# Optimization experiments

Hardware: AMD Instinct MI355X
Metric: run time of the kernel (lower is better)

Reference implementation:

```python
import jax, jax.numpy as jnp
import numpy as np

NDIM = 3
N = 192
DX = 1.0 / N          # uniform unit box
T_REF = 300.0         # reference temperature [K]
MU_REF = 1.8e-5       # reference viscosity [Pa s]
PR = 0.72             # Prandtl number
CP = 1005.0           # specific heat [J/kg/K]


def _ddx(f, axis):
    # 2nd-order central difference, periodic BC
    return (jnp.roll(f, -1, axis) - jnp.roll(f, 1, axis)) / (2.0 * DX)


def _gradient(f):
    # scalar [N,N,N] -> [NDIM, N,N,N]
    return jnp.stack([_ddx(f, a) for a in range(NDIM)], axis=0)


def _divergence(v):
    # vector [NDIM, N,N,N] -> [N,N,N]
    out = _ddx(v[0], 0)
    for a in range(1, NDIM):
        out = out + _ddx(v[a], a)
    return out


def _viscosity(T_dim):
    return MU_REF * (T_dim / T_REF) ** 0.7


def _conductivity(T_dim):
    return _viscosity(T_dim) * CP / PR


def setup_inputs() -> dict:
    key = jax.random.key(0)
    k1, k2 = jax.random.split(key)
    u = jax.random.normal(k1, (NDIM, N, N, N), dtype=jnp.float32)
    # nondimensional temperature, kept positive for the power-law viscosity
    T = jax.random.uniform(k2, (N, N, N), dtype=jnp.float32, minval=0.5, maxval=1.5)
    return {"u": u, "T": T}


def reference(u, T):
    # --- stress tensor ---
    mu = _viscosity(T * T_REF)                                   # [N,N,N]
    # gradu[i, j] = d u_i / d x_j
    gradu = jnp.stack([_gradient(u[i]) for i in range(NDIM)], 0)  # [3,3,N,N,N]
    divu = jnp.einsum('ii...->...', gradu)                        # trace -> [N,N,N]
    S = 0.5 * (gradu + jnp.swapaxes(gradu, 0, 1))                 # symmetrized
    eye = jnp.eye(NDIM, dtype=u.dtype)[:, :, None, None, None]
    tau = 2.0 * mu * S - (2.0 / 3.0) * mu * divu * eye            # [3,3,N,N,N]

    # --- heat flux ---
    k = _conductivity(T * T_REF)
    heat_flux = -k * _gradient(T)                                 # [3,N,N,N]

    # --- assemble RHS: [mass(=0), momentum(3), energy] ---
    momentum = jnp.stack([_divergence(tau[i]) for i in range(NDIM)], 0)
    energy = -_divergence(heat_flux)
    for i in range(NDIM):
        energy = energy + _divergence(tau[i] * u[i])
    zero = jnp.zeros_like(T)
    return jnp.concatenate([zero[None], momentum, energy[None]], axis=0)
```

## Files before the change

### kernel.cpp

```cpp
#include <hip/hip_runtime.h>

#define N  192
#define N2 (N * N)
#define N3 (N * N * N)

#define TX 32
#define TY 8
#define NT 256
#define ZC 12
#define GX (N / TX)
#define GY (N / TY)
#define GZ (N / ZC)
#define NBLK (GX * GY * GZ)
#define UX (TX + 4)
#define UY (TY + 4)
#define UP (UX * UY)
#define FX (TX + 2)
#define FY (TY + 2)
#define FP (FX * FY)

static constexpr float INV2DX     = (float)N / 2.0f;
static constexpr float MU_REF_F   = 1.8e-5f;
static constexpr float CP_OVER_PR = 1005.0f / 0.72f;
static constexpr float TWO_THIRDS = 2.0f / 3.0f;

__device__ __forceinline__ int wrapN(int a) {
    if (a < 0)  a += N;
    if (a >= N) a -= N;
    return a;
}

struct Flux { float t00, t01, t02, t11, t12, t22, F0, F1, F2; };

__device__ __forceinline__ Flux flux_eval(const float4* __restrict__ uM,
                                          const float4* __restrict__ uC,
                                          const float4* __restrict__ uP,
                                          int c)
{
    const float4 cc = uC[c];
    const float4 xp = uC[c + 1],  xm = uC[c - 1];
    const float4 yp = uC[c + UX], ym = uC[c - UX];
    const float4 zp = uP[c],      zm = uM[c];

    const float d00 = (zp.x - zm.x) * INV2DX;
    const float d01 = (yp.x - ym.x) * INV2DX;
    const float d02 = (xp.x - xm.x) * INV2DX;
    const float d10 = (zp.y - zm.y) * INV2DX;
    const float d11 = (yp.y - ym.y) * INV2DX;
    const float d12 = (xp.y - xm.y) * INV2DX;
    const float d20 = (zp.z - zm.z) * INV2DX;
    const float d21 = (yp.z - ym.z) * INV2DX;
    const float d22 = (xp.z - xm.z) * INV2DX;
    const float dT0 = (zp.w - zm.w) * INV2DX;
    const float dT1 = (yp.w - ym.w) * INV2DX;
    const float dT2 = (xp.w - xm.w) * INV2DX;

    const float mu   = MU_REF_F * __powf(cc.w, 0.7f);
    const float divu = d00 + d11 + d22;
    const float lam  = -TWO_THIRDS * mu * divu;

    Flux f;
    f.t00 = 2.0f * mu * d00 + lam;
    f.t11 = 2.0f * mu * d11 + lam;
    f.t22 = 2.0f * mu * d22 + lam;
    f.t01 = mu * (d01 + d10);
    f.t02 = mu * (d02 + d20);
    f.t12 = mu * (d12 + d21);
    const float kc = mu * CP_OVER_PR;
    f.F0 = kc * dT0 + f.t00 * cc.x + f.t01 * cc.y + f.t02 * cc.z;
    f.F1 = kc * dT1 + f.t01 * cc.x + f.t11 * cc.y + f.t12 * cc.z;
    f.F2 = kc * dT2 + f.t02 * cc.x + f.t12 * cc.y + f.t22 * cc.z;
    return f;
}

__device__ __forceinline__ void sf_store(float4* __restrict__ sA, float4* __restrict__ sB,
                                         int fi, const Flux& f)
{
    sA[fi] = make_float4(f.t01, f.t02, f.t11, f.t12);
    sB[fi] = make_float4(f.t22, f.F1,  f.F2,  0.0f);
}

__global__ __launch_bounds__(NT)
void diffusion_zmarch_kernel(const float* __restrict__ u,
                             const float* __restrict__ Tp,
                             float* __restrict__ out)
{
    __shared__ float4 su4[4][UP];
    __shared__ float4 sfA[2][FP];
    __shared__ float4 sfB[2][FP];

    const int id  = (int)blockIdx.x;
    const int nid = (id & 7) * (NBLK / 8) + (id >> 3);
    const int bzB = nid / (GX * GY);
    const int rem = nid % (GX * GY);
    const int bx  = (rem % GX) * TX;
    const int by  = (rem / GX) * TY;
    const int z0  = bzB * ZC;

    const int tx  = threadIdx.x & (TX - 1);
    const int ty  = threadIdx.x >> 5;
    const int tid = (int)threadIdx.x;

    const float* __restrict__ u0 = u;
    const float* __restrict__ u1 = u + N3;
    const float* __restrict__ u2 = u + 2 * N3;

    const int cu = (ty + 2) * UX + (tx + 2);
    const int fi = (ty + 1) * FX + (tx + 1);

    int hfx = -1, hfy = -1;
    if (tid < TX)                 { hfy = 0;      hfx = 1 + tid; }
    else if (tid < 2 * TX)        { hfy = FY - 1; hfx = 1 + tid - TX; }
    else if (tid < 2 * TX + TY)   { hfx = 0;      hfy = 1 + tid - 2 * TX; }
    else if (tid < 2 * (TX + TY)) { hfx = FX - 1; hfy = 1 + tid - 2 * TX - TY; }
    const int hcu = (hfy + 1) * UX + (hfx + 1);
    const int hfi = hfy * FX + hfx;

    const int  q0   = tid;
    const int  q1   = tid + NT;
    const bool has2 = (q1 < UP);
    int ro0, ro1 = 0;
    {
        const int ux = q0 % UX, uy = q0 / UX;
        ro0 = wrapN(by + uy - 2) * N + wrapN(bx + ux - 2);
    }
    if (has2) {
        const int ux = q1 % UX, uy = q1 / UX;
        ro1 = wrapN(by + uy - 2) * N + wrapN(bx + ux - 2);
    }

#define STAGE_DIRECT(slot, zw)                                              \
    do {                                                                    \
        const int base_ = (zw) * N2;                                        \
        {  const int g_ = base_ + ro0;                                      \
           su4[slot][q0] = make_float4(u0[g_], u1[g_], u2[g_], Tp[g_]); }   \
        if (has2) {                                                         \
           const int g_ = base_ + ro1;                                      \
           su4[slot][q1] = make_float4(u0[g_], u1[g_], u2[g_], Tp[g_]); }   \
    } while (0)

    STAGE_DIRECT(0, wrapN(z0 - 2));
    STAGE_DIRECT(1, wrapN(z0 - 1));
    STAGE_DIRECT(2, z0);
    STAGE_DIRECT(3, z0 + 1);
    __syncthreads();

    float t00m, t01m, t02m, F0m;
    float t00c, t01c, t02c, F0c;
    {
        const Flux fM = flux_eval(su4[0], su4[1], su4[2], cu);
        t00m = fM.t00; t01m = fM.t01; t02m = fM.t02; F0m = fM.F0;
        const Flux fC = flux_eval(su4[1], su4[2], su4[3], cu);
        t00c = fC.t00; t01c = fC.t01; t02c = fC.t02; F0c = fC.F0;
        sf_store(sfA[0], sfB[0], fi, fC);
        if (hfx >= 0) {
            const Flux h = flux_eval(su4[1], su4[2], su4[3], hcu);
            sf_store(sfA[0], sfB[0], hfi, h);
        }
    }
    __syncthreads();
    STAGE_DIRECT(0, z0 + 2);
    __syncthreads();

    float4 *pM = su4[2], *pC = su4[3], *pP = su4[0], *pW = su4[1];
    int cur = 1;
    const int obase = (by + ty) * N + bx + tx;

    for (int z = z0; z < z0 + ZC; ++z) {
        const bool pref = (z <= z0 + ZC - 2);
        float4 r0, r1;
        if (pref) {
            int zw = z + 3; if (zw >= N) zw -= N;
            const int base_ = zw * N2;
            { const int g_ = base_ + ro0;
              r0 = make_float4(u0[g_], u1[g_], u2[g_], Tp[g_]); }
            if (has2) {
              const int g_ = base_ + ro1;
              r1 = make_float4(u0[g_], u1[g_], u2[g_], Tp[g_]); }
        }

        const Flux fp_ = flux_eval(pM, pC, pP, cu);
        Flux h;
        if (hfx >= 0) h = flux_eval(pM, pC, pP, hcu);

        const float4* __restrict__ sA = sfA[cur ^ 1];
        const float4* __restrict__ sB = sfB[cur ^ 1];
        const float4 ayp = sA[fi + FX], aym = sA[fi - FX];
        const float4 axp = sA[fi + 1],  axm = sA[fi - 1];
        const float4 byp = sB[fi + FX], bym = sB[fi - FX];
        const float4 bxp = sB[fi + 1],  bxm = sB[fi - 1];

        const float m0 = (fp_.t00 - t00m) + (ayp.x - aym.x) + (axp.y - axm.y);
        const float m1 = (fp_.t01 - t01m) + (ayp.z - aym.z) + (axp.w - axm.w);
        const float m2 = (fp_.t02 - t02m) + (ayp.w - aym.w) + (bxp.x - bxm.x);
        const float en = (fp_.F0  - F0m)  + (byp.y - bym.y) + (bxp.z - bxm.z);

        const int idx = z * N2 + obase;
        out[idx]          = 0.0f;
        out[1 * N3 + idx] = m0 * INV2DX;
        out[2 * N3 + idx] = m1 * INV2DX;
        out[3 * N3 + idx] = m2 * INV2DX;
        out[4 * N3 + idx] = en * INV2DX;

        if (pref) { pW[q0] = r0; if (has2) pW[q1] = r1; }
        sf_store(sfA[cur], sfB[cur], fi, fp_);
        if (hfx >= 0) sf_store(sfA[cur], sfB[cur], hfi, h);

        __syncthreads();

        t00m = t00c; t01m = t01c; t02m = t02c; F0m = F0c;
        t00c = fp_.t00; t01c = fp_.t01; t02c = fp_.t02; F0c = fp_.F0;
        float4* t = pM; pM = pC; pC = pP; pP = pW; pW = t;
        cur ^= 1;
    }
#undef STAGE_DIRECT
}

extern "C" void kernel_launch(void* const* d_in, const int* in_sizes, int n_in,
                              void* d_out, int out_size, void* d_ws, size_t ws_size,
                              hipStream_t stream)
{
    const float* u   = (const float*)d_in[0];
    const float* T   = (const float*)d_in[1];
    float*       out = (float*)d_out;

    hipLaunchKernelGGL(diffusion_zmarch_kernel, dim3(NBLK), dim3(NT), 0, stream,
                       u, T, out);
}
```

Before: 106.2 us.

## Cut shared memory to three plane buffers and single flux buffer, pad rows

```diff
diff --git a/kernel.cpp b/kernel.cpp
--- a/kernel.cpp
+++ b/kernel.cpp
@@ -12,12 +12,17 @@
 #define GY (N / TY)
 #define GZ (N / ZC)
 #define NBLK (GX * GY * GZ)
-#define UX (TX + 4)
-#define UY (TY + 4)
-#define UP (UX * UY)
-#define FX (TX + 2)
-#define FY (TY + 2)
-#define FP (FX * FY)
+
+#define UXS 36
+#define UY  12
+#define UXP 37
+#define UP  (UXS * UY)
+#define UPP (UXP * UY)
+
+#define FXS 34
+#define FY  10
+#define FXP 35
+#define FPP (FXP * FY)
 
 static constexpr float INV2DX     = (float)N / 2.0f;
 static constexpr float MU_REF_F   = 1.8e-5f;
@@ -38,9 +43,9 @@
                                           int c)
 {
     const float4 cc = uC[c];
-    const float4 xp = uC[c + 1],  xm = uC[c - 1];
-    const float4 yp = uC[c + UX], ym = uC[c - UX];
-    const float4 zp = uP[c],      zm = uM[c];
+    const float4 xp = uC[c + 1],   xm = uC[c - 1];
+    const float4 yp = uC[c + UXP], ym = uC[c - UXP];
+    const float4 zp = uP[c],       zm = uM[c];
 
     const float d00 = (zp.x - zm.x) * INV2DX;
     const float d01 = (yp.x - ym.x) * INV2DX;
@@ -73,21 +78,14 @@
     return f;
 }
 
-__device__ __forceinline__ void sf_store(float4* __restrict__ sA, float4* __restrict__ sB,
-                                         int fi, const Flux& f)
-{
-    sA[fi] = make_float4(f.t01, f.t02, f.t11, f.t12);
-    sB[fi] = make_float4(f.t22, f.F1,  f.F2,  0.0f);
-}
-
-__global__ __launch_bounds__(NT)
+__global__ __launch_bounds__(NT, 5)
 void diffusion_zmarch_kernel(const float* __restrict__ u,
                              const float* __restrict__ Tp,
                              float* __restrict__ out)
 {
-    __shared__ float4 su4[4][UP];
-    __shared__ float4 sfA[2][FP];
-    __shared__ float4 sfB[2][FP];
+    __shared__ float4 su4[3][UPP];
+    __shared__ float4 sfA[FPP];
+    __shared__ float4 sfB[FPP];
 
     const int id  = (int)blockIdx.x;
     const int nid = (id & 7) * (NBLK / 8) + (id >> 3);
@@ -105,72 +103,80 @@
     const float* __restrict__ u1 = u + N3;
     const float* __restrict__ u2 = u + 2 * N3;
 
-    const int cu = (ty + 2) * UX + (tx + 2);
-    const int fi = (ty + 1) * FX + (tx + 1);
+    const int cu = (ty + 2) * UXP + (tx + 2);
+    const int fi = (ty + 1) * FXP + (tx + 1);
 
     int hfx = -1, hfy = -1;
-    if (tid < TX)                 { hfy = 0;      hfx = 1 + tid; }
-    else if (tid < 2 * TX)        { hfy = FY - 1; hfx = 1 + tid - TX; }
-    else if (tid < 2 * TX + TY)   { hfx = 0;      hfy = 1 + tid - 2 * TX; }
-    else if (tid < 2 * (TX + TY)) { hfx = FX - 1; hfy = 1 + tid - 2 * TX - TY; }
-    const int hcu = (hfy + 1) * UX + (hfx + 1);
-    const int hfi = hfy * FX + hfx;
+    if (tid < TX)                 { hfy = 0;       hfx = 1 + tid; }
+    else if (tid < 2 * TX)        { hfy = FY - 1;  hfx = 1 + tid - TX; }
+    else if (tid < 2 * TX + TY)   { hfx = 0;       hfy = 1 + tid - 2 * TX; }
+    else if (tid < 2 * (TX + TY)) { hfx = FXS - 1; hfy = 1 + tid - 2 * TX - TY; }
+    const int hcu = (hfy + 1) * UXP + (hfx + 1);
+    const int hfi = hfy * FXP + hfx;
 
     const int  q0   = tid;
     const int  q1   = tid + NT;
     const bool has2 = (q1 < UP);
-    int ro0, ro1 = 0;
+    int ro0, ro1 = 0, p0, p1 = 0;
     {
-        const int ux = q0 % UX, uy = q0 / UX;
+        const int ux = q0 % UXS, uy = q0 / UXS;
         ro0 = wrapN(by + uy - 2) * N + wrapN(bx + ux - 2);
+        p0  = uy * UXP + ux;
     }
     if (has2) {
-        const int ux = q1 % UX, uy = q1 / UX;
+        const int ux = q1 % UXS, uy = q1 / UXS;
         ro1 = wrapN(by + uy - 2) * N + wrapN(bx + ux - 2);
+        p1  = uy * UXP + ux;
     }
 
 #define STAGE_DIRECT(slot, zw)                                              \
     do {                                                                    \
         const int base_ = (zw) * N2;                                        \
         {  const int g_ = base_ + ro0;                                      \
-           su4[slot][q0] = make_float4(u0[g_], u1[g_], u2[g_], Tp[g_]); }   \
+           su4[slot][p0] = make_float4(u0[g_], u1[g_], u2[g_], Tp[g_]); }   \
         if (has2) {                                                         \
            const int g_ = base_ + ro1;                                      \
-           su4[slot][q1] = make_float4(u0[g_], u1[g_], u2[g_], Tp[g_]); }   \
+           su4[slot][p1] = make_float4(u0[g_], u1[g_], u2[g_], Tp[g_]); }   \
     } while (0)
 
     STAGE_DIRECT(0, wrapN(z0 - 2));
     STAGE_DIRECT(1, wrapN(z0 - 1));
     STAGE_DIRECT(2, z0);
-    STAGE_DIRECT(3, z0 + 1);
     __syncthreads();
 
     float t00m, t01m, t02m, F0m;
-    float t00c, t01c, t02c, F0c;
     {
         const Flux fM = flux_eval(su4[0], su4[1], su4[2], cu);
         t00m = fM.t00; t01m = fM.t01; t02m = fM.t02; F0m = fM.F0;
-        const Flux fC = flux_eval(su4[1], su4[2], su4[3], cu);
+    }
+    __syncthreads();
+    STAGE_DIRECT(0, z0 + 1);
+    __syncthreads();
+
+    float t00c, t01c, t02c, F0c;
+    {
+        const Flux fC = flux_eval(su4[1], su4[2], su4[0], cu);
         t00c = fC.t00; t01c = fC.t01; t02c = fC.t02; F0c = fC.F0;
-        sf_store(sfA[0], sfB[0], fi, fC);
+        sfA[fi] = make_float4(fC.t01, fC.t02, fC.t11, fC.t12);
+        sfB[fi] = make_float4(fC.t22, fC.F1, fC.F2, 0.0f);
         if (hfx >= 0) {
-            const Flux h = flux_eval(su4[1], su4[2], su4[3], hcu);
-            sf_store(sfA[0], sfB[0], hfi, h);
+            const Flux h = flux_eval(su4[1], su4[2], su4[0], hcu);
+            sfA[hfi] = make_float4(h.t01, h.t02, h.t11, h.t12);
+            sfB[hfi] = make_float4(h.t22, h.F1, h.F2, 0.0f);
         }
     }
     __syncthreads();
-    STAGE_DIRECT(0, z0 + 2);
-    __syncthreads();
-
-    float4 *pM = su4[2], *pC = su4[3], *pP = su4[0], *pW = su4[1];
-    int cur = 1;
+    STAGE_DIRECT(1, z0 + 2);
+    __syncthreads();
+
+    float4 *pM = su4[2], *pC = su4[0], *pP = su4[1];
     const int obase = (by + ty) * N + bx + tx;
 
     for (int z = z0; z < z0 + ZC; ++z) {
         const bool pref = (z <= z0 + ZC - 2);
         float4 r0, r1;
         if (pref) {
-            int zw = z + 3; if (zw >= N) zw -= N;
+            const int zw = wrapN(z + 3);
             const int base_ = zw * N2;
             { const int g_ = base_ + ro0;
               r0 = make_float4(u0[g_], u1[g_], u2[g_], Tp[g_]); }
@@ -183,12 +189,10 @@
         Flux h;
         if (hfx >= 0) h = flux_eval(pM, pC, pP, hcu);
 
-        const float4* __restrict__ sA = sfA[cur ^ 1];
-        const float4* __restrict__ sB = sfB[cur ^ 1];
-        const float4 ayp = sA[fi + FX], aym = sA[fi - FX];
-        const float4 axp = sA[fi + 1],  axm = sA[fi - 1];
-        const float4 byp = sB[fi + FX], bym = sB[fi - FX];
-        const float4 bxp = sB[fi + 1],  bxm = sB[fi - 1];
+        const float4 ayp = sfA[fi + FXP], aym = sfA[fi - FXP];
+        const float4 axp = sfA[fi + 1],   axm = sfA[fi - 1];
+        const float4 byp = sfB[fi + FXP], bym = sfB[fi - FXP];
+        const float4 bxp = sfB[fi + 1],   bxm = sfB[fi - 1];
 
         const float m0 = (fp_.t00 - t00m) + (ayp.x - aym.x) + (axp.y - axm.y);
         const float m1 = (fp_.t01 - t01m) + (ayp.z - aym.z) + (axp.w - axm.w);
@@ -202,16 +206,21 @@
         out[3 * N3 + idx] = m2 * INV2DX;
         out[4 * N3 + idx] = en * INV2DX;
 
-        if (pref) { pW[q0] = r0; if (has2) pW[q1] = r1; }
-        sf_store(sfA[cur], sfB[cur], fi, fp_);
-        if (hfx >= 0) sf_store(sfA[cur], sfB[cur], hfi, h);
+        __syncthreads();
+
+        if (pref) { pM[p0] = r0; if (has2) pM[p1] = r1; }
+        sfA[fi] = make_float4(fp_.t01, fp_.t02, fp_.t11, fp_.t12);
+        sfB[fi] = make_float4(fp_.t22, fp_.F1, fp_.F2, 0.0f);
+        if (hfx >= 0) {
+            sfA[hfi] = make_float4(h.t01, h.t02, h.t11, h.t12);
+            sfB[hfi] = make_float4(h.t22, h.F1, h.F2, 0.0f);
+        }
 
         __syncthreads();
 
         t00m = t00c; t01m = t01c; t02m = t02c; F0m = F0c;
         t00c = fp_.t00; t01c = fp_.t01; t02c = fp_.t02; F0c = fp_.F0;
-        float4* t = pM; pM = pC; pC = pP; pP = pW; pW = t;
-        cur ^= 1;
+        float4* t = pM; pM = pC; pC = pP; pP = t;
     }
 #undef STAGE_DIRECT
 }
```

Result: slower. 134.3 us (+26.4%).
